# Kernel optimization log

Hardware: AMD Instinct MI355X
Metric: run time of the kernel (lower is better)

The kernel has to match this reference:

```python
import jax, jax.numpy as jnp
import numpy as np


def setup_inputs() -> dict:
    key = jax.random.key(0)
    ks = jax.random.split(key, 8)
    B, W, H, C = 4, 64, 64, 256
    C2 = C // 2
    s = 0.05
    x = jax.random.normal(ks[0], (B, W, H, C), dtype=jnp.float32)
    Wq = jax.random.normal(ks[1], (C, C2), dtype=jnp.float32) * s
    bq = jax.random.normal(ks[2], (C2,), dtype=jnp.float32) * s
    Wk = jax.random.normal(ks[3], (C, C2), dtype=jnp.float32) * s
    bk = jax.random.normal(ks[4], (C2,), dtype=jnp.float32) * s
    Wv = jax.random.normal(ks[5], (C, C), dtype=jnp.float32) * s
    bv = jax.random.normal(ks[6], (C,), dtype=jnp.float32) * s
    # gamma is initialized to 0 in the original; use a nonzero value so the
    # attention branch actually contributes (math is identical).
    gamma = jnp.array([0.5], dtype=jnp.float32)
    return {"x": x, "Wq": Wq, "bq": bq, "Wk": Wk, "bk": bk, "Wv": Wv, "bv": bv, "gamma": gamma}


def reference(x, Wq, bq, Wk, bk, Wv, bv, gamma):
    B, W, H, C = x.shape
    N = W * H
    # 1x1 convs == per-pixel linear projections
    q = jnp.einsum('bwhc,cd->bwhd', x, Wq) + bq   # [B,W,H,C/2]
    k = jnp.einsum('bwhc,cd->bwhd', x, Wk) + bk   # [B,W,H,C/2]
    v = jnp.einsum('bwhc,cd->bwhd', x, Wv) + bv   # [B,W,H,C]
    # Faithful to original: raw row-major reshape (B,W,H,Cq) -> (B,Cq,N)
    # (this mixes spatial and channel axes, exactly as the TF code does)
    pq = q.reshape(B, -1, N)                      # [B,C/2,N]
    pk = k.reshape(B, -1, N)                      # [B,C/2,N]
    pv = v.reshape(B, -1, N)                      # [B,C,N]
    energy = jnp.einsum('bcn,bcm->bnm', pq, pk)   # [B,N,N] (pq transposed)
    attention = jax.nn.softmax(energy, axis=-1)   # [B,N,N]
    out = jnp.einsum('bcm,bnm->bcn', pv, attention)  # pv @ attention^T
    out = out.reshape(B, W, H, C)
    return gamma * out + x
```

## Files before the change

kernel.cpp:

```cpp
#include <hip/hip_runtime.h>
#include <hip/hip_bf16.h>
#include <stdint.h>


typedef __attribute__((ext_vector_type(8)))  short short8;
typedef __attribute__((ext_vector_type(4)))  float f32x4;
typedef __attribute__((ext_vector_type(16))) float f32x16;
typedef __attribute__((ext_vector_type(4)))  unsigned short u16x4;

#define MFMA16 __builtin_amdgcn_mfma_f32_16x16x32_bf16
#define MFMA32 __builtin_amdgcn_mfma_f32_32x32x16_bf16

__device__ __forceinline__ unsigned short f2bf(float f) {
    union { float f; uint32_t u; } v; v.f = f;
    return (unsigned short)((v.u + 0x8000u) >> 16);
}
__device__ __forceinline__ float bf2f(unsigned short h) {
    union { uint32_t u; float f; } v; v.u = ((uint32_t)h) << 16;
    return v.f;
}
__device__ __forceinline__ uint32_t pkbf(float a, float b) {
    union { __hip_bfloat162 h; uint32_t u; } v;
    v.h = __float22bfloat162_rn(float2{a, b});
    return v.u;
}

__global__ void prep_w(const float* __restrict__ Wq, const float* __restrict__ bq,
                       const float* __restrict__ Wk, const float* __restrict__ bk,
                       const float* __restrict__ Wv, const float* __restrict__ bv,
                       unsigned short* __restrict__ Wt, float* __restrict__ bias) {
    int g = blockIdx.x * 256 + threadIdx.x;
    int c = g & 255, d = g >> 8;
    float val;
    if (d < 128)      val = Wq[c * 128 + d];
    else if (d < 256) val = Wk[c * 128 + (d - 128)];
    else              val = Wv[c * 256 + (d - 256)];
    Wt[d * 256 + c] = f2bf(val);
    if (g < 512) {
        float bb;
        if (g < 128)      bb = bq[g];
        else if (g < 256) bb = bk[g - 128];
        else              bb = bv[g - 256];
        bias[g] = bb;
    }
}

__global__ __launch_bounds__(256) void proj(
        const float* __restrict__ x, const unsigned short* __restrict__ Wt,
        const float* __restrict__ bias,
        unsigned short* __restrict__ Qrm, unsigned short* __restrict__ Kp,
        unsigned short* __restrict__ Vp) {
    __shared__ unsigned short T[128 * 136];
    int bid = blockIdx.x;
    int tid = threadIdx.x;
    int wave = tid >> 6, lane = tid & 63;
    int l16 = lane & 15, quad = lane >> 4;

    int kind, b, a, vh = 0;
    if (bid < 256) { kind = bid >> 7; int s = bid & 127; b = s >> 5; a = s & 31; }
    else           { kind = 2; int s = bid - 256; vh = s >> 7; b = (s >> 5) & 3; a = s & 31; }

    short8 af[2][8];
    #pragma unroll
    for (int g = 0; g < 2; ++g) {
        int p_local = wave * 32 + g * 16 + l16;
        int pix = (kind == 2) ? (b * 4096 + a * 128 + p_local)
                              : (b * 4096 + a + 32 * p_local);
        const float* xr = x + (size_t)pix * 256;
        #pragma unroll
        for (int kk = 0; kk < 8; ++kk) {
            f32x4 u0 = *(const f32x4*)(xr + kk * 32 + quad * 8);
            f32x4 u1 = *(const f32x4*)(xr + kk * 32 + quad * 8 + 4);
            union { short8 s; uint32_t u[4]; } h;
            h.u[0] = pkbf(u0[0], u0[1]); h.u[1] = pkbf(u0[2], u0[3]);
            h.u[2] = pkbf(u1[0], u1[1]); h.u[3] = pkbf(u1[2], u1[3]);
            af[g][kk] = h.s;
        }
    }

    if (kind < 2) {
        int dbase = kind * 128;
        #pragma unroll 1
        for (int dt = 0; dt < 8; ++dt) {
            int d = dbase + dt * 16 + l16;
            float bval = bias[d];
            f32x4 acc0 = {0.f,0.f,0.f,0.f}, acc1 = {0.f,0.f,0.f,0.f};
            #pragma unroll
            for (int kk = 0; kk < 8; ++kk) {
                short8 wrow = *(const short8*)(Wt + d * 256 + kk * 32 + quad * 8);
                acc0 = MFMA16(af[0][kk], wrow, acc0, 0, 0, 0);
                acc1 = MFMA16(af[1][kk], wrow, acc1, 0, 0, 0);
            }
            #pragma unroll
            for (int g = 0; g < 2; ++g) {
                f32x4 acc = g ? acc1 : acc0;
                union { u16x4 v; uint32_t u[2]; } pk;
                pk.u[0] = pkbf(acc[0] + bval, acc[1] + bval);
                pk.u[1] = pkbf(acc[2] + bval, acc[3] + bval);
                *(u16x4*)(T + (dt * 16 + l16) * 136 + wave * 32 + g * 16 + quad * 4) = pk.v;
            }
        }
        __syncthreads();
        if (kind == 0) {
            unsigned short* ob = Qrm + (b << 19) + a * 128 * 128;
            #pragma unroll
            for (int it = 0; it < 8; ++it) {
                int ci = it * 256 + tid;
                int row = ci >> 4, cj = ci & 15;
                *(short8*)(ob + row * 128 + cj * 8) = *(const short8*)(T + row * 136 + cj * 8);
            }
        } else {
            unsigned short* kb = Kp + (b << 19);
            #pragma unroll
            for (int it = 0; it < 8; ++it) {
                int ci = it * 256 + tid;
                int row = ci >> 4, cj = ci & 15;
                *(short8*)(kb + (cj >> 1) * 65536 + (a * 128 + row) * 16 + (cj & 1) * 8)
                    = *(const short8*)(T + row * 136 + cj * 8);
            }
        }
    } else {
        #pragma unroll 1
        for (int dt = 0; dt < 8; ++dt) {
            int d = 256 + vh * 128 + dt * 16 + l16;
            f32x4 acc0 = {0.f,0.f,0.f,0.f}, acc1 = {0.f,0.f,0.f,0.f};
            #pragma unroll
            for (int kk = 0; kk < 8; ++kk) {
                short8 wrow = *(const short8*)(Wt + d * 256 + kk * 32 + quad * 8);
                acc0 = MFMA16(wrow, af[0][kk], acc0, 0, 0, 0);
                acc1 = MFMA16(wrow, af[1][kk], acc1, 0, 0, 0);
            }
            int dvl = dt * 16 + quad * 4;
            f32x4 bv4 = *(const f32x4*)(bias + 256 + vh * 128 + dvl);
            #pragma unroll
            for (int g = 0; g < 2; ++g) {
                f32x4 acc = g ? acc1 : acc0;
                union { u16x4 v; uint32_t u[2]; } pk;
                pk.u[0] = pkbf(acc[0] + bv4[0], acc[1] + bv4[1]);
                pk.u[1] = pkbf(acc[2] + bv4[2], acc[3] + bv4[3]);
                int p_local = wave * 32 + g * 16 + l16;
                *(u16x4*)(T + p_local * 136 + dvl) = pk.v;
            }
        }
        __syncthreads();
        unsigned short* vb = Vp + (b << 20);
        #pragma unroll
        for (int it = 0; it < 8; ++it) {
            int cid = it * 256 + tid;
            int c_local = cid >> 8, w = cid & 255;
            int p_local = c_local * 16 + (w >> 4);
            int chunk = (w >> 4) * 16 + vh * 8 + ((w & 15) >> 1);
            *(short8*)(vb + chunk * 4096 + (a * 8 + c_local) * 16 + (w & 1) * 8)
                = *(const short8*)(T + p_local * 136 + (w & 15) * 8);
        }
    }
}

__global__ __launch_bounds__(256, 2) void attn(
        const unsigned short* __restrict__ Qrm, const unsigned short* __restrict__ Kp,
        const unsigned short* __restrict__ Vp, unsigned short* __restrict__ Opart,
        float* __restrict__ Lpart) {
    __shared__ unsigned short Ps[2 * 64 * 72];

    int bid = blockIdx.x;
    int comb = bid & 7, qt = bid >> 3;
    int b = comb >> 1, ks = comb & 1;
    int tid = threadIdx.x, wave = tid >> 6, lane = tid & 63;
    int l32 = lane & 31, half = lane >> 5;
    int mt = wave & 1, nt = wave >> 1;

    const unsigned short* Qb = Qrm + (b << 19);
    const unsigned short* Kb = Kp + (b << 19);
    const unsigned short* Vb = Vp + (b << 20);

    int q0 = qt * 64;

    short8 qf[8];
    {
        const unsigned short* qrow = Qb + (q0 + nt * 32 + l32) * 128 + half * 8;
        #pragma unroll
        for (int kk = 0; kk < 8; ++kk) qf[kk] = *(const short8*)(qrow + kk * 16);
    }

    f32x16 O[2][2];
    #pragma unroll
    for (int i = 0; i < 2; ++i)
        #pragma unroll
        for (int j = 0; j < 2; ++j)
            #pragma unroll
            for (int r = 0; r < 16; ++r) O[i][j][r] = 0.f;
    float l_run = 0.f;

    const int m_base = ks * 2048;
    const int chunk_base = ks * 128;
    const int kbase = (m_base + mt * 32 + l32) * 16 + half * 8;

    short8 kf[8];
    #pragma unroll
    for (int kk = 0; kk < 8; ++kk)
        kf[kk] = *(const short8*)(Kb + kk * 65536 + kbase);
    short8 vfrag[2][4];
    #pragma unroll
    for (int c2 = 0; c2 < 2; ++c2)
        #pragma unroll
        for (int k2 = 0; k2 < 4; ++k2)
            vfrag[c2][k2] = *(const short8*)(Vb + (chunk_base + k2) * 4096
                              + ((wave * 2 + c2) * 32 + l32) * 16 + half * 8);
    {
        f32x16 S;
        #pragma unroll
        for (int r = 0; r < 16; ++r) S[r] = 0.f;
        #pragma unroll
        for (int kk = 0; kk < 8; ++kk) S = MFMA32(kf[kk], qf[kk], S, 0, 0, 0);
        #pragma unroll
        for (int g = 0; g < 4; ++g) {
            float p0 = __expf(S[g * 4 + 0]), p1 = __expf(S[g * 4 + 1]);
            float p2 = __expf(S[g * 4 + 2]), p3 = __expf(S[g * 4 + 3]);
            l_run += (p0 + p1) + (p2 + p3);
            union { u16x4 v; uint32_t u[2]; } pk;
            pk.u[0] = pkbf(p0, p1); pk.u[1] = pkbf(p2, p3);
            *(u16x4*)(Ps + (nt * 32 + l32) * 72 + mt * 32 + g * 8 + half * 4) = pk.v;
        }
        #pragma unroll
        for (int kk = 0; kk < 8; ++kk)
            kf[kk] = *(const short8*)(Kb + kk * 65536 + 64 * 16 + kbase);
    }

    #pragma unroll 1
    for (int kt = 0; kt < 32; ++kt) {
        __syncthreads();

        if (kt < 31) {
            f32x16 S;
            #pragma unroll
            for (int r = 0; r < 16; ++r) S[r] = 0.f;
            #pragma unroll
            for (int kk = 0; kk < 8; ++kk) S = MFMA32(kf[kk], qf[kk], S, 0, 0, 0);
            if (kt < 30) {
                int kr = (kt + 2) * 64 * 16 + kbase;
                #pragma unroll
                for (int kk = 0; kk < 8; ++kk)
                    kf[kk] = *(const short8*)(Kb + kk * 65536 + kr);
            }
            unsigned short* Pn = Ps + ((kt + 1) & 1) * (64 * 72);
            #pragma unroll
            for (int g = 0; g < 4; ++g) {
                float p0 = __expf(S[g * 4 + 0]), p1 = __expf(S[g * 4 + 1]);
                float p2 = __expf(S[g * 4 + 2]), p3 = __expf(S[g * 4 + 3]);
                l_run += (p0 + p1) + (p2 + p3);
                union { u16x4 v; uint32_t u[2]; } pk;
                pk.u[0] = pkbf(p0, p1); pk.u[1] = pkbf(p2, p3);
                *(u16x4*)(Pn + (nt * 32 + l32) * 72 + mt * 32 + g * 8 + half * 4) = pk.v;
            }
        }

        unsigned short* Pb = Ps + (kt & 1) * (64 * 72);
        #pragma unroll
        for (int k2 = 0; k2 < 4; ++k2) {
            short8 pa0 = *(const short8*)(Pb + (l32) * 72 + k2 * 16 + half * 8);
            short8 pa1 = *(const short8*)(Pb + (32 + l32) * 72 + k2 * 16 + half * 8);
            O[0][0] = MFMA32(pa0, vfrag[0][k2], O[0][0], 0, 0, 0);
            O[0][1] = MFMA32(pa0, vfrag[1][k2], O[0][1], 0, 0, 0);
            O[1][0] = MFMA32(pa1, vfrag[0][k2], O[1][0], 0, 0, 0);
            O[1][1] = MFMA32(pa1, vfrag[1][k2], O[1][1], 0, 0, 0);
        }

        if (kt < 31) {
            int ch1 = chunk_base + (kt + 1) * 4;
            #pragma unroll
            for (int c2 = 0; c2 < 2; ++c2)
                #pragma unroll
                for (int k2 = 0; k2 < 4; ++k2)
                    vfrag[c2][k2] = *(const short8*)(Vb + (ch1 + k2) * 4096
                                      + ((wave * 2 + c2) * 32 + l32) * 16 + half * 8);
        }
    }

    l_run += __shfl_xor(l_run, 32);
    unsigned short* Op = Opart + ((size_t)(ks * 4 + b) << 20);
    #pragma unroll
    for (int q2 = 0; q2 < 2; ++q2)
        #pragma unroll
        for (int c2 = 0; c2 < 2; ++c2) {
            int c = (wave * 2 + c2) * 32 + l32;
            #pragma unroll
            for (int r = 0; r < 16; ++r) {
                int n = q0 + q2 * 32 + (r & 3) + 8 * (r >> 2) + 4 * half;
                Op[(size_t)n * 256 + c] = f2bf(O[q2][c2][r]);
            }
        }
    if (half == 0) {
        int n = q0 + nt * 32 + l32;
        Lpart[((ks * 2 + mt) * 4 + b) * 4096 + n] = l_run;
    }
}

__global__ __launch_bounds__(256) void merge_out(
        const unsigned short* __restrict__ Opart, const float* __restrict__ Lpart,
        const float* __restrict__ x, const float* __restrict__ gamma,
        float* __restrict__ out) {
    __shared__ float tile[64 * 257];
    __shared__ float wsm[64];
    int b  = blockIdx.x >> 6;
    int n0 = (blockIdx.x & 63) << 6;
    int tid = threadIdx.x;
    float g = gamma[0];
    if (tid < 64) {
        int n = n0 + tid;
        float L = 0.f;
        #pragma unroll
        for (int s = 0; s < 4; ++s) L += Lpart[(s * 4 + b) * 4096 + n];
        wsm[tid] = g / L;
    }
    __syncthreads();
    int nl1 = tid >> 5, cb1 = (tid & 31) * 8;
    const unsigned short* Op0 = Opart + ((size_t)b << 20);
    const unsigned short* Op1 = Opart + ((size_t)(4 + b) << 20);
    #pragma unroll
    for (int i = 0; i < 8; ++i) {
        int nl = i * 8 + nl1;
        size_t off = (size_t)(n0 + nl) * 256 + cb1;
        short8 o0 = *(const short8*)(Op0 + off);
        short8 o1 = *(const short8*)(Op1 + off);
        float w = wsm[nl];
        float* tr = tile + nl * 257 + cb1;
        #pragma unroll
        for (int e = 0; e < 8; ++e)
            tr[e] = (bf2f((unsigned short)o0[e]) + bf2f((unsigned short)o1[e])) * w;
    }
    __syncthreads();
    int cg = tid >> 4, nq = (tid & 15) * 4;
    #pragma unroll
    for (int it = 0; it < 16; ++it) {
        int c = it * 16 + cg;
        size_t idx = ((size_t)b << 20) + (size_t)c * 4096 + n0 + nq;
        f32x4 xv = *(const f32x4*)(x + idx);
        f32x4 ov;
        #pragma unroll
        for (int e = 0; e < 4; ++e) ov[e] = tile[(nq + e) * 257 + c] + xv[e];
        *(f32x4*)(out + idx) = ov;
    }
}

extern "C" void kernel_launch(void* const* d_in, const int* in_sizes, int n_in,
                              void* d_out, int out_size, void* d_ws, size_t ws_size,
                              hipStream_t stream) {
    const float* x     = (const float*)d_in[0];
    const float* Wq    = (const float*)d_in[1];
    const float* bq    = (const float*)d_in[2];
    const float* Wk    = (const float*)d_in[3];
    const float* bk    = (const float*)d_in[4];
    const float* Wv    = (const float*)d_in[5];
    const float* bv    = (const float*)d_in[6];
    const float* gamma = (const float*)d_in[7];
    float* out = (float*)d_out;

    if (ws_size < 34080768u) return;

    char* ws = (char*)d_ws;
    unsigned short* Wt    = (unsigned short*)(ws);
    float*          bias  = (float*)        (ws +   262144);
    unsigned short* Qrm   = (unsigned short*)(ws +   264192);
    unsigned short* Kp    = (unsigned short*)(ws +  4458496);
    unsigned short* Vp    = (unsigned short*)(ws +  8652800);
    unsigned short* Opart = (unsigned short*)(ws + 17041408);
    float*          Lpart = (float*)        (ws + 33818624);

    prep_w   <<<512, 256, 0, stream>>>(Wq, bq, Wk, bk, Wv, bv, Wt, bias);
    proj     <<<512, 256, 0, stream>>>(x, Wt, bias, Qrm, Kp, Vp);
    attn     <<<512, 256, 0, stream>>>(Qrm, Kp, Vp, Opart, Lpart);
    merge_out<<<256, 256, 0, stream>>>(Opart, Lpart, x, gamma, out);
}
```

Measured before the change: 170.9 us.

## Process two key tiles per barrier with quad-buffered P tiles in LDS

The attention main loop now handles two 64-key tiles per iteration and uses four LDS buffers for the softmax probability tiles instead of two. This halves the number of __syncthreads barriers and interleaves the QK MFMAs, exp work and PV MFMAs of neighbouring tiles so more independent work sits between loads and their use. In exchange, LDS use per block doubles, which may reduce occupancy, and register pressure rises from holding two score accumulators at once.

```diff
diff --git a/kernel.cpp b/kernel.cpp
--- a/kernel.cpp
+++ b/kernel.cpp
@@ -160,7 +160,7 @@
         const unsigned short* __restrict__ Qrm, const unsigned short* __restrict__ Kp,
         const unsigned short* __restrict__ Vp, unsigned short* __restrict__ Opart,
         float* __restrict__ Lpart) {
-    __shared__ unsigned short Ps[2 * 64 * 72];
+    __shared__ unsigned short Ps[4 * 64 * 72];
 
     int bid = blockIdx.x;
     int comb = bid & 7, qt = bid >> 3;
@@ -206,12 +206,14 @@
         for (int k2 = 0; k2 < 4; ++k2)
             vfrag[c2][k2] = *(const short8*)(Vb + (chunk_base + k2) * 4096
                               + ((wave * 2 + c2) * 32 + l32) * 16 + half * 8);
-    {
+    #pragma unroll 1
+    for (int pt = 0; pt < 2; ++pt) {
         f32x16 S;
         #pragma unroll
         for (int r = 0; r < 16; ++r) S[r] = 0.f;
         #pragma unroll
         for (int kk = 0; kk < 8; ++kk) S = MFMA32(kf[kk], qf[kk], S, 0, 0, 0);
+        unsigned short* Pn = Ps + pt * (64 * 72);
         #pragma unroll
         for (int g = 0; g < 4; ++g) {
             float p0 = __expf(S[g * 4 + 0]), p1 = __expf(S[g * 4 + 1]);
@@ -219,60 +221,115 @@
             l_run += (p0 + p1) + (p2 + p3);
             union { u16x4 v; uint32_t u[2]; } pk;
             pk.u[0] = pkbf(p0, p1); pk.u[1] = pkbf(p2, p3);
-            *(u16x4*)(Ps + (nt * 32 + l32) * 72 + mt * 32 + g * 8 + half * 4) = pk.v;
+            *(u16x4*)(Pn + (nt * 32 + l32) * 72 + mt * 32 + g * 8 + half * 4) = pk.v;
         }
         #pragma unroll
         for (int kk = 0; kk < 8; ++kk)
-            kf[kk] = *(const short8*)(Kb + kk * 65536 + 64 * 16 + kbase);
+            kf[kk] = *(const short8*)(Kb + kk * 65536 + (pt + 1) * 64 * 16 + kbase);
     }
 
     #pragma unroll 1
-    for (int kt = 0; kt < 32; ++kt) {
+    for (int e = 0; e < 16; ++e) {
         __syncthreads();
-
-        if (kt < 31) {
-            f32x16 S;
-            #pragma unroll
-            for (int r = 0; r < 16; ++r) S[r] = 0.f;
-            #pragma unroll
-            for (int kk = 0; kk < 8; ++kk) S = MFMA32(kf[kk], qf[kk], S, 0, 0, 0);
-            if (kt < 30) {
-                int kr = (kt + 2) * 64 * 16 + kbase;
-                #pragma unroll
-                for (int kk = 0; kk < 8; ++kk)
-                    kf[kk] = *(const short8*)(Kb + kk * 65536 + kr);
-            }
-            unsigned short* Pn = Ps + ((kt + 1) & 1) * (64 * 72);
-            #pragma unroll
-            for (int g = 0; g < 4; ++g) {
-                float p0 = __expf(S[g * 4 + 0]), p1 = __expf(S[g * 4 + 1]);
-                float p2 = __expf(S[g * 4 + 2]), p3 = __expf(S[g * 4 + 3]);
-                l_run += (p0 + p1) + (p2 + p3);
-                union { u16x4 v; uint32_t u[2]; } pk;
-                pk.u[0] = pkbf(p0, p1); pk.u[1] = pkbf(p2, p3);
-                *(u16x4*)(Pn + (nt * 32 + l32) * 72 + mt * 32 + g * 8 + half * 4) = pk.v;
-            }
-        }
-
-        unsigned short* Pb = Ps + (kt & 1) * (64 * 72);
-        #pragma unroll
-        for (int k2 = 0; k2 < 4; ++k2) {
-            short8 pa0 = *(const short8*)(Pb + (l32) * 72 + k2 * 16 + half * 8);
-            short8 pa1 = *(const short8*)(Pb + (32 + l32) * 72 + k2 * 16 + half * 8);
-            O[0][0] = MFMA32(pa0, vfrag[0][k2], O[0][0], 0, 0, 0);
-            O[0][1] = MFMA32(pa0, vfrag[1][k2], O[0][1], 0, 0, 0);
-            O[1][0] = MFMA32(pa1, vfrag[0][k2], O[1][0], 0, 0, 0);
-            O[1][1] = MFMA32(pa1, vfrag[1][k2], O[1][1], 0, 0, 0);
-        }
-
-        if (kt < 31) {
-            int ch1 = chunk_base + (kt + 1) * 4;
+        const int t0 = 2 * e;
+
+        f32x16 SA;
+        if (e < 15) {
+            #pragma unroll
+            for (int r = 0; r < 16; ++r) SA[r] = 0.f;
+            #pragma unroll
+            for (int kk = 0; kk < 8; ++kk) SA = MFMA32(kf[kk], qf[kk], SA, 0, 0, 0);
+            int kr = (t0 + 3) * 64 * 16 + kbase;
+            #pragma unroll
+            for (int kk = 0; kk < 8; ++kk)
+                kf[kk] = *(const short8*)(Kb + kk * 65536 + kr);
+        }
+
+        {
+            unsigned short* Pb = Ps + (t0 & 3) * (64 * 72);
+            #pragma unroll
+            for (int k2 = 0; k2 < 4; ++k2) {
+                short8 pa0 = *(const short8*)(Pb + (l32) * 72 + k2 * 16 + half * 8);
+                short8 pa1 = *(const short8*)(Pb + (32 + l32) * 72 + k2 * 16 + half * 8);
+                O[0][0] = MFMA32(pa0, vfrag[0][k2], O[0][0], 0, 0, 0);
+                O[0][1] = MFMA32(pa0, vfrag[1][k2], O[0][1], 0, 0, 0);
+                O[1][0] = MFMA32(pa1, vfrag[0][k2], O[1][0], 0, 0, 0);
+                O[1][1] = MFMA32(pa1, vfrag[1][k2], O[1][1], 0, 0, 0);
+            }
+        }
+
+        {
+            int ch1 = chunk_base + (t0 + 1) * 4;
             #pragma unroll
             for (int c2 = 0; c2 < 2; ++c2)
                 #pragma unroll
                 for (int k2 = 0; k2 < 4; ++k2)
                     vfrag[c2][k2] = *(const short8*)(Vb + (ch1 + k2) * 4096
                                       + ((wave * 2 + c2) * 32 + l32) * 16 + half * 8);
+        }
+
+        if (e < 15) {
+            unsigned short* Pn = Ps + ((t0 + 2) & 3) * (64 * 72);
+            #pragma unroll
+            for (int g = 0; g < 4; ++g) {
+                float p0 = __expf(SA[g * 4 + 0]), p1 = __expf(SA[g * 4 + 1]);
+                float p2 = __expf(SA[g * 4 + 2]), p3 = __expf(SA[g * 4 + 3]);
+                l_run += (p0 + p1) + (p2 + p3);
+                union { u16x4 v; uint32_t u[2]; } pk;
+                pk.u[0] = pkbf(p0, p1); pk.u[1] = pkbf(p2, p3);
+                *(u16x4*)(Pn + (nt * 32 + l32) * 72 + mt * 32 + g * 8 + half * 4) = pk.v;
+            }
+        }
+
+        f32x16 SB;
+        if (e < 15) {
+            #pragma unroll
+            for (int r = 0; r < 16; ++r) SB[r] = 0.f;
+            #pragma unroll
+            for (int kk = 0; kk < 8; ++kk) SB = MFMA32(kf[kk], qf[kk], SB, 0, 0, 0);
+        }
+
+        {
+            unsigned short* Pb = Ps + ((t0 + 1) & 3) * (64 * 72);
+            #pragma unroll
+            for (int k2 = 0; k2 < 4; ++k2) {
+                short8 pa0 = *(const short8*)(Pb + (l32) * 72 + k2 * 16 + half * 8);
+                short8 pa1 = *(const short8*)(Pb + (32 + l32) * 72 + k2 * 16 + half * 8);
+                O[0][0] = MFMA32(pa0, vfrag[0][k2], O[0][0], 0, 0, 0);
+                O[0][1] = MFMA32(pa0, vfrag[1][k2], O[0][1], 0, 0, 0);
+                O[1][0] = MFMA32(pa1, vfrag[0][k2], O[1][0], 0, 0, 0);
+                O[1][1] = MFMA32(pa1, vfrag[1][k2], O[1][1], 0, 0, 0);
+            }
+        }
+
+        if (e < 15) {
+            int ch1 = chunk_base + (t0 + 2) * 4;
+            #pragma unroll
+            for (int c2 = 0; c2 < 2; ++c2)
+                #pragma unroll
+                for (int k2 = 0; k2 < 4; ++k2)
+                    vfrag[c2][k2] = *(const short8*)(Vb + (ch1 + k2) * 4096
+                                      + ((wave * 2 + c2) * 32 + l32) * 16 + half * 8);
+        }
+
+        if (e < 15) {
+            unsigned short* Pn = Ps + ((t0 + 3) & 3) * (64 * 72);
+            #pragma unroll
+            for (int g = 0; g < 4; ++g) {
+                float p0 = __expf(SB[g * 4 + 0]), p1 = __expf(SB[g * 4 + 1]);
+                float p2 = __expf(SB[g * 4 + 2]), p3 = __expf(SB[g * 4 + 3]);
+                l_run += (p0 + p1) + (p2 + p3);
+                union { u16x4 v; uint32_t u[2]; } pk;
+                pk.u[0] = pkbf(p0, p1); pk.u[1] = pkbf(p2, p3);
+                *(u16x4*)(Pn + (nt * 32 + l32) * 72 + mt * 32 + g * 8 + half * 4) = pk.v;
+            }
+        }
+
+        if (e < 14) {
+            int kr = (t0 + 4) * 64 * 16 + kbase;
+            #pragma unroll
+            for (int kk = 0; kk < 8; ++kk)
+                kf[kk] = *(const short8*)(Kb + kk * 65536 + kr);
         }
     }
 
```

Measured after the change: 172.2 us. No clear change (+0.8%).
